# Optimization experiments

Hardware: AMD Instinct MI355X
Metric: run time of the kernel (lower is better)

The kernel has to match this reference:

```python
import jax, jax.numpy as jnp
import numpy as np

B, V, NV, NR, N, E, D, H, OUT, L = 4, 20, 8000, 200, 8000, 200000, 128, 128, 64, 3
DECAY = 0.03


def setup_inputs() -> dict:
    key = jax.random.key(0)
    ks = jax.random.split(key, 16)
    node_ids = jax.random.randint(ks[0], (N,), 0, NV)
    rel_ids = jax.random.randint(ks[1], (E,), 0, NR)
    edge_index = jax.random.randint(ks[2], (2, E), 0, N)
    batch = jnp.repeat(jnp.arange(B), N // B)  # sorted graph assignment, 2000 nodes/graph
    visit_node = (jax.random.uniform(ks[3], (B, V, NV)) < 0.3).astype(jnp.float32)
    ehr_nodes = (jax.random.uniform(ks[4], (B, NV)) < 0.1).astype(jnp.float32)
    s = lambda k, shape: jax.random.normal(k, shape, jnp.float32) * 0.05
    return dict(
        node_ids=node_ids, rel_ids=rel_ids, edge_index=edge_index, batch=batch,
        visit_node=visit_node, ehr_nodes=ehr_nodes,
        node_emb_w=s(ks[5], (NV, D)), rel_emb_w=s(ks[6], (NR, D)),
        lin_w=s(ks[7], (D, H)), lin_b=jnp.zeros((H,), jnp.float32),
        alpha_w=s(ks[8], (L, H)), alpha_b=jnp.zeros((L,), jnp.float32),
        beta_w=s(ks[9], (L, NV)), beta_b=jnp.zeros((L,), jnp.float32),
        conv_w=s(ks[10], (L, H, H)), conv_b=jnp.zeros((L, H), jnp.float32),
        wr_w=s(ks[11], (L, H)), wr_b=jnp.zeros((L,), jnp.float32),
        mlp_w=s(ks[12], (2 * H, OUT)), mlp_b=jnp.zeros((OUT,), jnp.float32),
    )


def reference(node_ids, rel_ids, edge_index, batch, visit_node, ehr_nodes,
              node_emb_w, rel_emb_w, lin_w, lin_b, alpha_w, alpha_b,
              beta_w, beta_b, conv_w, conv_b, wr_w, wr_b, mlp_w, mlp_b):
    # shared input projection (torch: self.lin applied to node and edge embeddings)
    x = node_emb_w[node_ids] @ lin_w + lin_b          # [N,H]
    edge_attr = rel_emb_w[rel_ids] @ lin_w + lin_b    # [E,H]

    # pack per-graph node features into dense [B, NV, H] (x_new in torch, fixed across layers)
    counts = jax.ops.segment_sum(jnp.ones((N,), jnp.float32), batch, B)            # [B]
    starts = jnp.concatenate([jnp.zeros((1,), jnp.int32),
                              jnp.cumsum(counts.astype(jnp.int32))[:-1]])
    local = jnp.arange(N) - starts[batch]                                          # position within graph
    x_pad = jnp.zeros((B, NV, H), jnp.float32).at[batch, local].set(x)

    lam = jnp.exp(DECAY * (V - jnp.arange(V, dtype=jnp.float32)))[None, :, None]   # [1,V,1]
    src, dst = edge_index[0], edge_index[1]
    eb, en = batch[src], node_ids[src]

    for l in range(L):
        # alpha attention over visits (softmax on visit axis)
        feat = visit_node[..., None] * x_pad[:, None]                              # [B,V,NV,H]
        alpha = jax.nn.softmax(jnp.einsum('bvnh,h->bvn', feat, alpha_w[l]) + alpha_b[l], axis=1)
        # beta: time-decayed visit attention
        beta = jnp.tanh(visit_node @ beta_w[l] + beta_b[l])[:, :, None] * lam      # [B,V,1]
        attn_full = alpha * beta                                                   # [B,V,NV]
        attn_e = attn_full[eb, 0, en][:, None]                                     # [E,1] (visit idx 0 as in source)
        # BiAttentionGNNConv: gather-mul-relu-scatter with edge attention
        w_rel = (edge_attr @ wr_w[l] + wr_b[l])[:, None]                           # [E,1]
        msg = jax.nn.relu(x[src] * attn_e + w_rel * edge_attr)                     # [E,H]
        agg = jax.ops.segment_sum(msg, dst, N)                                     # scatter-add to targets
        x = jax.nn.relu((agg + x) @ conv_w[l] + conv_b[l])                         # eps=0 -> (1+eps)*x = x; dropout=eval

    # joint patient representation
    x_graph = jax.ops.segment_sum(x, batch, B) / counts[:, None]                   # global mean pool
    x_node = (ehr_nodes @ node_emb_w) / jnp.sum(ehr_nodes, axis=1, keepdims=True)  # [B,D]
    x_node = x_node @ lin_w + lin_b
    logits = jnp.concatenate([x_graph, x_node], axis=1) @ mlp_w + mlp_b            # [B,OUT]
    return logits
```

## Files before the change

kernel.cpp:

```cpp
#include <hip/hip_runtime.h>

#define NN  8000
#define EE  200000
#define BB  4
#define VV  20
#define NVV 8000
#define NRR 200
#define HH  128
#define OO  64
#define LL  3

__global__ void k_zero_small(float* p, int n) {
  int i = blockIdx.x * 256 + threadIdx.x;
  if (i < n) p[i] = 0.f;
}
__global__ void k_zero_int(int* p, int n) {
  int i = blockIdx.x * 256 + threadIdx.x;
  if (i < n) p[i] = 0;
}

__global__ __launch_bounds__(128) void k_proj_nodes(
    const int* __restrict__ node_ids, const float* __restrict__ emb,
    const float* __restrict__ lin_w, const float* __restrict__ lin_b,
    const float* __restrict__ alpha_w, float* __restrict__ x,
    float* __restrict__ snode)
{
  int i = blockIdx.x, t = threadIdx.x;
  __shared__ float row[HH];
  __shared__ float part[LL][2];
  row[t] = emb[node_ids[i] * HH + t];
  __syncthreads();
  float acc = lin_b[t];
  #pragma unroll 4
  for (int d = 0; d < HH; ++d) acc += row[d] * lin_w[d * HH + t];
  x[i * HH + t] = acc;
  #pragma unroll
  for (int l = 0; l < LL; ++l) {
    float v = acc * alpha_w[l * HH + t];
    for (int off = 32; off > 0; off >>= 1) v += __shfl_down(v, off, 64);
    if ((t & 63) == 0) part[l][t >> 6] = v;
  }
  __syncthreads();
  if (t == 0) {
    #pragma unroll
    for (int l = 0; l < LL; ++l) snode[l * NN + i] = part[l][0] + part[l][1];
  }
}

__global__ __launch_bounds__(128) void k_proj_rels(
    const float* __restrict__ rel_emb, const float* __restrict__ lin_w,
    const float* __restrict__ lin_b, const float* __restrict__ wr_w,
    const float* __restrict__ wr_b, float* __restrict__ relp,
    float* __restrict__ reldot)
{
  int r = blockIdx.x, t = threadIdx.x;
  __shared__ float row[HH];
  __shared__ float part[LL][2];
  row[t] = rel_emb[r * HH + t];
  __syncthreads();
  float acc = lin_b[t];
  #pragma unroll 4
  for (int d = 0; d < HH; ++d) acc += row[d] * lin_w[d * HH + t];
  relp[r * HH + t] = acc;
  #pragma unroll
  for (int l = 0; l < LL; ++l) {
    float v = acc * wr_w[l * HH + t];
    for (int off = 32; off > 0; off >>= 1) v += __shfl_down(v, off, 64);
    if ((t & 63) == 0) part[l][t >> 6] = v;
  }
  __syncthreads();
  if (t == 0) {
    #pragma unroll
    for (int l = 0; l < LL; ++l) reldot[l * NRR + r] = part[l][0] + part[l][1] + wr_b[l];
  }
}

__global__ __launch_bounds__(256) void k_beta(
    const float* __restrict__ visit_node, const float* __restrict__ beta_w,
    const float* __restrict__ beta_b, float* __restrict__ beta0)
{
  int l = blockIdx.x >> 2, b = blockIdx.x & 3, t = threadIdx.x;
  __shared__ float red[256];
  float acc = 0.f;
  for (int n = t; n < NVV; n += 256)
    acc += visit_node[(b * VV + 0) * NVV + n] * beta_w[l * NVV + n];
  red[t] = acc;
  __syncthreads();
  for (int s = 128; s > 0; s >>= 1) {
    if (t < s) red[t] += red[t + s];
    __syncthreads();
  }
  if (t == 0) beta0[l * BB + b] = tanhf(red[0] + beta_b[l]) * expf(0.03f * 20.0f);
}

__global__ __launch_bounds__(256) void k_attn(
    const float* __restrict__ visit_node, const float* __restrict__ snode,
    const float* __restrict__ alpha_b, const float* __restrict__ beta0,
    float* __restrict__ attn0)
{
  int idx = blockIdx.x * 256 + threadIdx.x;
  if (idx >= BB * NVV) return;
  int b = idx / NVV, n = idx % NVV;
  float vn[VV];
  #pragma unroll
  for (int v = 0; v < VV; ++v) vn[v] = visit_node[(b * VV + v) * NVV + n];
  for (int l = 0; l < LL; ++l) {
    float s = (n < NN / BB) ? snode[l * NN + b * (NN / BB) + n] : 0.0f;
    float ab = alpha_b[l];
    float m = -1e30f;
    #pragma unroll
    for (int v = 0; v < VV; ++v) m = fmaxf(m, vn[v] * s + ab);
    float sum = 0.f;
    #pragma unroll
    for (int v = 0; v < VV; ++v) sum += expf(vn[v] * s + ab - m);
    float a0 = expf(vn[0] * s + ab - m) / sum;
    attn0[(l * BB + b) * NVV + n] = a0 * beta0[l * BB + b];
  }
}

__global__ void k_anode(const int* __restrict__ node_ids, const int* __restrict__ batch,
                        const float* __restrict__ attn0, float* __restrict__ anode)
{
  int i = blockIdx.x * 256 + threadIdx.x;
  if (i >= NN) return;
  int b = batch[i], nid = node_ids[i];
  #pragma unroll
  for (int l = 0; l < LL; ++l) anode[l * NN + i] = attn0[(l * BB + b) * NVV + nid];
}

__global__ void k_hist(const int* __restrict__ edge_index, int* __restrict__ deg) {
  int e = blockIdx.x * 256 + threadIdx.x;
  if (e >= EE) return;
  atomicAdd(&deg[edge_index[EE + e]], 1);
}

__global__ __launch_bounds__(1024) void k_scan(const int* __restrict__ deg,
                                               int* __restrict__ row_ptr)
{
  int t = threadIdx.x;
  __shared__ int ps[1024];
  int local[8];
  int base = t * 8;
  int s = 0;
  #pragma unroll
  for (int j = 0; j < 8; ++j) {
    int idx = base + j;
    int v = (idx < NN) ? deg[idx] : 0;
    local[j] = s; s += v;
  }
  ps[t] = s;
  __syncthreads();
  for (int off = 1; off < 1024; off <<= 1) {
    int v = (t >= off) ? ps[t - off] : 0;
    __syncthreads();
    ps[t] += v;
    __syncthreads();
  }
  int excl = (t == 0) ? 0 : ps[t - 1];
  #pragma unroll
  for (int j = 0; j < 8; ++j) {
    int idx = base + j;
    if (idx < NN) row_ptr[idx] = excl + local[j];
  }
  if (t == 1023) row_ptr[NN] = ps[1023];
}

__global__ void k_scatter(const int* __restrict__ edge_index, const int* __restrict__ rel_ids,
                          const int* __restrict__ row_ptr, int* __restrict__ cursor,
                          int* __restrict__ csr_src, int* __restrict__ csr_rid)
{
  int e = blockIdx.x * 256 + threadIdx.x;
  if (e >= EE) return;
  int dst = edge_index[EE + e];
  int p = row_ptr[dst] + atomicAdd(&cursor[dst], 1);
  csr_src[p] = edge_index[e];
  csr_rid[p] = rel_ids[e];
}

__global__ __launch_bounds__(128) void k_gather_conv(
    const int* __restrict__ row_ptr, const int* __restrict__ csr_src,
    const int* __restrict__ csr_rid, const float* __restrict__ xin,
    const float* __restrict__ relp, const float* __restrict__ anode,
    const float* __restrict__ reldot, const float* __restrict__ conv_w,
    const float* __restrict__ conv_b, float* __restrict__ xout, int l)
{
  int i = blockIdx.x, t = threadIdx.x;
  __shared__ float wl[NRR];
  __shared__ float aggrow[HH];
  for (int r = t; r < NRR; r += HH) wl[r] = reldot[l * NRR + r];
  __syncthreads();
  float acc = xin[i * HH + t];
  int k0 = row_ptr[i], k1 = row_ptr[i + 1];
  for (int k = k0; k < k1; ++k) {
    int src = csr_src[k];
    int rid = csr_rid[k];
    float a = anode[l * NN + src];
    acc += fmaxf(xin[src * HH + t] * a + wl[rid] * relp[rid * HH + t], 0.f);
  }
  aggrow[t] = acc;
  __syncthreads();
  float o = conv_b[l * HH + t];
  #pragma unroll 4
  for (int d = 0; d < HH; ++d) o += aggrow[d] * conv_w[(l * HH + d) * HH + t];
  xout[i * HH + t] = fmaxf(o, 0.f);
}

__global__ __launch_bounds__(128) void k_xgraph(
    const float* __restrict__ x, float* __restrict__ xg_raw)
{
  int b = blockIdx.x >> 4, c = blockIdx.x & 15, t = threadIdx.x;
  const int per = (NN / BB) / 16;
  int base = b * (NN / BB) + c * per;
  float acc = 0.f;
  for (int i = 0; i < per; ++i) acc += x[(base + i) * HH + t];
  atomicAdd(&xg_raw[b * HH + t], acc);
}

__global__ __launch_bounds__(128) void k_xnode(
    const float* __restrict__ ehr, const float* __restrict__ emb,
    float* __restrict__ xn_raw, float* __restrict__ denom)
{
  int b = blockIdx.x >> 5, c = blockIdx.x & 31, t = threadIdx.x;
  const int per = NVV / 32;
  int base = c * per;
  float acc = 0.f;
  for (int n = base; n < base + per; ++n)
    acc += ehr[b * NVV + n] * emb[n * HH + t];
  atomicAdd(&xn_raw[b * HH + t], acc);
  __shared__ float red[128];
  float dsum = 0.f;
  for (int n = base + t; n < base + per; n += 128) dsum += ehr[b * NVV + n];
  red[t] = dsum;
  __syncthreads();
  for (int s = 64; s > 0; s >>= 1) {
    if (t < s) red[t] += red[t + s];
    __syncthreads();
  }
  if (t == 0) atomicAdd(&denom[b], red[0]);
}

__global__ __launch_bounds__(128) void k_final(
    const float* __restrict__ xg_raw, const float* __restrict__ xn_raw,
    const float* __restrict__ denom, const float* __restrict__ lin_w,
    const float* __restrict__ lin_b, const float* __restrict__ mlp_w,
    const float* __restrict__ mlp_b, float* __restrict__ out)
{
  int b = blockIdx.x, t = threadIdx.x;
  __shared__ float xg[HH], xn[HH], xnp[HH];
  xg[t] = xg_raw[b * HH + t] * (1.0f / (NN / BB));
  xn[t] = xn_raw[b * HH + t] / denom[b];
  __syncthreads();
  float a3 = lin_b[t];
  #pragma unroll 4
  for (int d = 0; d < HH; ++d) a3 += xn[d] * lin_w[d * HH + t];
  xnp[t] = a3;
  __syncthreads();
  if (t < OO) {
    float a4 = mlp_b[t];
    #pragma unroll 4
    for (int h = 0; h < HH; ++h)
      a4 += xg[h] * mlp_w[h * OO + t] + xnp[h] * mlp_w[(HH + h) * OO + t];
    out[b * OO + t] = a4;
  }
}

extern "C" void kernel_launch(void* const* d_in, const int* in_sizes, int n_in,
                              void* d_out, int out_size, void* d_ws, size_t ws_size,
                              hipStream_t stream) {
  const int*   node_ids   = (const int*)d_in[0];
  const int*   rel_ids    = (const int*)d_in[1];
  const int*   edge_index = (const int*)d_in[2];
  const int*   batch      = (const int*)d_in[3];
  const float* visit_node = (const float*)d_in[4];
  const float* ehr        = (const float*)d_in[5];
  const float* node_emb   = (const float*)d_in[6];
  const float* rel_emb    = (const float*)d_in[7];
  const float* lin_w      = (const float*)d_in[8];
  const float* lin_b      = (const float*)d_in[9];
  const float* alpha_w    = (const float*)d_in[10];
  const float* alpha_b    = (const float*)d_in[11];
  const float* beta_w     = (const float*)d_in[12];
  const float* beta_b     = (const float*)d_in[13];
  const float* conv_w     = (const float*)d_in[14];
  const float* conv_b     = (const float*)d_in[15];
  const float* wr_w       = (const float*)d_in[16];
  const float* wr_b       = (const float*)d_in[17];
  const float* mlp_w      = (const float*)d_in[18];
  const float* mlp_b      = (const float*)d_in[19];
  float* out = (float*)d_out;

  float* ws = (float*)d_ws;
  float* xA     = ws; ws += NN * HH;
  float* xB     = ws; ws += NN * HH;
  float* relp   = ws; ws += NRR * HH;
  float* reldot = ws; ws += LL * NRR;
  float* snode  = ws; ws += LL * NN;
  float* beta0  = ws; ws += LL * BB;
  float* attn0  = ws; ws += LL * BB * NVV;
  float* anode  = ws; ws += LL * NN;
  float* xg_raw = ws; ws += BB * HH;
  float* xn_raw = ws; ws += BB * HH;
  float* denom  = ws; ws += BB;
  int* iws      = (int*)ws;
  int* deg      = iws; iws += NN;
  int* cursor   = iws; iws += NN;
  int* row_ptr  = iws; iws += NN + 1;
  int* csr_src  = iws; iws += EE;
  int* csr_rid  = iws; iws += EE;

  int nsmall = BB * HH * 2 + BB;
  hipLaunchKernelGGL(k_zero_small, dim3((nsmall + 255) / 256), dim3(256), 0, stream,
                     xg_raw, nsmall);
  hipLaunchKernelGGL(k_zero_int, dim3((2 * NN + 255) / 256), dim3(256), 0, stream,
                     deg, 2 * NN);

  hipLaunchKernelGGL(k_proj_nodes, dim3(NN), dim3(HH), 0, stream,
                     node_ids, node_emb, lin_w, lin_b, alpha_w, xA, snode);
  hipLaunchKernelGGL(k_proj_rels, dim3(NRR), dim3(HH), 0, stream,
                     rel_emb, lin_w, lin_b, wr_w, wr_b, relp, reldot);
  hipLaunchKernelGGL(k_beta, dim3(LL * BB), dim3(256), 0, stream,
                     visit_node, beta_w, beta_b, beta0);
  hipLaunchKernelGGL(k_attn, dim3((BB * NVV + 255) / 256), dim3(256), 0, stream,
                     visit_node, snode, alpha_b, beta0, attn0);
  hipLaunchKernelGGL(k_anode, dim3((NN + 255) / 256), dim3(256), 0, stream,
                     node_ids, batch, attn0, anode);

  hipLaunchKernelGGL(k_hist, dim3((EE + 255) / 256), dim3(256), 0, stream,
                     edge_index, deg);
  hipLaunchKernelGGL(k_scan, dim3(1), dim3(1024), 0, stream, deg, row_ptr);
  hipLaunchKernelGGL(k_scatter, dim3((EE + 255) / 256), dim3(256), 0, stream,
                     edge_index, rel_ids, row_ptr, cursor, csr_src, csr_rid);

  const float* xin = xA;
  float* xout = xB;
  for (int l = 0; l < LL; ++l) {
    hipLaunchKernelGGL(k_gather_conv, dim3(NN), dim3(HH), 0, stream,
                       row_ptr, csr_src, csr_rid, xin, relp, anode, reldot,
                       conv_w, conv_b, xout, l);
    const float* tmp = xin; xin = xout; xout = (float*)tmp;
  }

  hipLaunchKernelGGL(k_xgraph, dim3(BB * 16), dim3(HH), 0, stream, xB, xg_raw);
  hipLaunchKernelGGL(k_xnode, dim3(BB * 32), dim3(HH), 0, stream,
                     ehr, node_emb, xn_raw, denom);
  hipLaunchKernelGGL(k_final, dim3(BB), dim3(HH), 0, stream,
                     xg_raw, xn_raw, denom, lin_w, lin_b, mlp_w, mlp_b, out);
}
```

Before: 358.9 us.

## Batch nodes per block, vectorize gather-conv, precompute per-edge attention and relation terms

The gather-conv kernel now handles 8 nodes per 256-thread block, with 32 lanes per node using float4 loads. The edge loop is unrolled by two, and the conv weights are reused across the 8 nodes. Relation terms are premultiplied per layer (wr·relp), and per-edge attention values are precomputed into CSR order during the scatter, which removes indirect loads from the inner loop. Node projection also processes 8 nodes per block to reuse lin_w, and the two zeroing kernels are merged. In exchange it uses more workspace and lowers the thread count per node, and the beta multiply moves into k_anode.

Result: faster. 320.7 us (-10.7%).

```diff
diff --git a/kernel.cpp b/kernel.cpp
--- a/kernel.cpp
+++ b/kernel.cpp
@@ -9,14 +9,12 @@
 #define HH  128
 #define OO  64
 #define LL  3
-
-__global__ void k_zero_small(float* p, int n) {
+#define NPB 8
+
+__global__ void k_zero(float* fz, int nf, int* iz, int ni) {
   int i = blockIdx.x * 256 + threadIdx.x;
-  if (i < n) p[i] = 0.f;
-}
-__global__ void k_zero_int(int* p, int n) {
-  int i = blockIdx.x * 256 + threadIdx.x;
-  if (i < n) p[i] = 0;
+  if (i < nf) fz[i] = 0.f;
+  if (i < ni) iz[i] = 0;
 }
 
 __global__ __launch_bounds__(128) void k_proj_nodes(
@@ -25,33 +23,55 @@
     const float* __restrict__ alpha_w, float* __restrict__ x,
     float* __restrict__ snode)
 {
-  int i = blockIdx.x, t = threadIdx.x;
-  __shared__ float row[HH];
-  __shared__ float part[LL][2];
-  row[t] = emb[node_ids[i] * HH + t];
-  __syncthreads();
-  float acc = lin_b[t];
-  #pragma unroll 4
-  for (int d = 0; d < HH; ++d) acc += row[d] * lin_w[d * HH + t];
-  x[i * HH + t] = acc;
+  int blk = blockIdx.x, t = threadIdx.x;
+  __shared__ float er[NPB][HH];
+  __shared__ float part[LL][NPB][2];
+  int base = blk * NPB;
+  #pragma unroll
+  for (int n = 0; n < NPB; ++n)
+    er[n][t] = emb[node_ids[base + n] * HH + t];
+  __syncthreads();
+  float bt = lin_b[t];
+  float acc[NPB];
+  #pragma unroll
+  for (int n = 0; n < NPB; ++n) acc[n] = bt;
+  for (int d4 = 0; d4 < HH / 4; ++d4) {
+    float e4[NPB][4];
+    #pragma unroll
+    for (int n = 0; n < NPB; ++n) {
+      float4 v = *(const float4*)&er[n][d4 * 4];
+      e4[n][0] = v.x; e4[n][1] = v.y; e4[n][2] = v.z; e4[n][3] = v.w;
+    }
+    #pragma unroll
+    for (int j = 0; j < 4; ++j) {
+      float lwv = lin_w[(d4 * 4 + j) * HH + t];
+      #pragma unroll
+      for (int n = 0; n < NPB; ++n) acc[n] += e4[n][j] * lwv;
+    }
+  }
+  #pragma unroll
+  for (int n = 0; n < NPB; ++n) x[(base + n) * HH + t] = acc[n];
   #pragma unroll
   for (int l = 0; l < LL; ++l) {
-    float v = acc * alpha_w[l * HH + t];
-    for (int off = 32; off > 0; off >>= 1) v += __shfl_down(v, off, 64);
-    if ((t & 63) == 0) part[l][t >> 6] = v;
-  }
-  __syncthreads();
-  if (t == 0) {
+    float aw = alpha_w[l * HH + t];
     #pragma unroll
-    for (int l = 0; l < LL; ++l) snode[l * NN + i] = part[l][0] + part[l][1];
+    for (int n = 0; n < NPB; ++n) {
+      float v = acc[n] * aw;
+      for (int off = 32; off > 0; off >>= 1) v += __shfl_down(v, off, 64);
+      if ((t & 63) == 0) part[l][n][t >> 6] = v;
+    }
+  }
+  __syncthreads();
+  if (t < LL * NPB) {
+    int l = t / NPB, n = t % NPB;
+    snode[l * NN + base + n] = part[l][n][0] + part[l][n][1];
   }
 }
 
 __global__ __launch_bounds__(128) void k_proj_rels(
     const float* __restrict__ rel_emb, const float* __restrict__ lin_w,
     const float* __restrict__ lin_b, const float* __restrict__ wr_w,
-    const float* __restrict__ wr_b, float* __restrict__ relp,
-    float* __restrict__ reldot)
+    const float* __restrict__ wr_b, float* __restrict__ wrelp)
 {
   int r = blockIdx.x, t = threadIdx.x;
   __shared__ float row[HH];
@@ -61,7 +81,6 @@
   float acc = lin_b[t];
   #pragma unroll 4
   for (int d = 0; d < HH; ++d) acc += row[d] * lin_w[d * HH + t];
-  relp[r * HH + t] = acc;
   #pragma unroll
   for (int l = 0; l < LL; ++l) {
     float v = acc * wr_w[l * HH + t];
@@ -69,9 +88,10 @@
     if ((t & 63) == 0) part[l][t >> 6] = v;
   }
   __syncthreads();
-  if (t == 0) {
-    #pragma unroll
-    for (int l = 0; l < LL; ++l) reldot[l * NRR + r] = part[l][0] + part[l][1] + wr_b[l];
+  #pragma unroll
+  for (int l = 0; l < LL; ++l) {
+    float rd = part[l][0] + part[l][1] + wr_b[l];
+    wrelp[(l * NRR + r) * HH + t] = rd * acc;
   }
 }
 
@@ -95,8 +115,7 @@
 
 __global__ __launch_bounds__(256) void k_attn(
     const float* __restrict__ visit_node, const float* __restrict__ snode,
-    const float* __restrict__ alpha_b, const float* __restrict__ beta0,
-    float* __restrict__ attn0)
+    const float* __restrict__ alpha_b, float* __restrict__ attn0)
 {
   int idx = blockIdx.x * 256 + threadIdx.x;
   if (idx >= BB * NVV) return;
@@ -113,19 +132,20 @@
     float sum = 0.f;
     #pragma unroll
     for (int v = 0; v < VV; ++v) sum += expf(vn[v] * s + ab - m);
-    float a0 = expf(vn[0] * s + ab - m) / sum;
-    attn0[(l * BB + b) * NVV + n] = a0 * beta0[l * BB + b];
+    attn0[(l * BB + b) * NVV + n] = expf(vn[0] * s + ab - m) / sum;
   }
 }
 
 __global__ void k_anode(const int* __restrict__ node_ids, const int* __restrict__ batch,
-                        const float* __restrict__ attn0, float* __restrict__ anode)
+                        const float* __restrict__ attn0, const float* __restrict__ beta0,
+                        float* __restrict__ anode)
 {
   int i = blockIdx.x * 256 + threadIdx.x;
   if (i >= NN) return;
   int b = batch[i], nid = node_ids[i];
   #pragma unroll
-  for (int l = 0; l < LL; ++l) anode[l * NN + i] = attn0[(l * BB + b) * NVV + nid];
+  for (int l = 0; l < LL; ++l)
+    anode[l * NN + i] = attn0[(l * BB + b) * NVV + nid] * beta0[l * BB + b];
 }
 
 __global__ void k_hist(const int* __restrict__ edge_index, int* __restrict__ deg) {
@@ -167,42 +187,80 @@
 
 __global__ void k_scatter(const int* __restrict__ edge_index, const int* __restrict__ rel_ids,
                           const int* __restrict__ row_ptr, int* __restrict__ cursor,
-                          int* __restrict__ csr_src, int* __restrict__ csr_rid)
+                          int2* __restrict__ csr_sr, float* __restrict__ csr_a,
+                          const float* __restrict__ anode)
 {
   int e = blockIdx.x * 256 + threadIdx.x;
   if (e >= EE) return;
+  int src = edge_index[e];
   int dst = edge_index[EE + e];
+  int rid = rel_ids[e];
   int p = row_ptr[dst] + atomicAdd(&cursor[dst], 1);
-  csr_src[p] = edge_index[e];
-  csr_rid[p] = rel_ids[e];
-}
-
-__global__ __launch_bounds__(128) void k_gather_conv(
-    const int* __restrict__ row_ptr, const int* __restrict__ csr_src,
-    const int* __restrict__ csr_rid, const float* __restrict__ xin,
-    const float* __restrict__ relp, const float* __restrict__ anode,
-    const float* __restrict__ reldot, const float* __restrict__ conv_w,
+  csr_sr[p] = make_int2(src, rid);
+  csr_a[0 * EE + p] = anode[0 * NN + src];
+  csr_a[1 * EE + p] = anode[1 * NN + src];
+  csr_a[2 * EE + p] = anode[2 * NN + src];
+}
+
+__global__ __launch_bounds__(256) void k_gather_conv(
+    const int* __restrict__ row_ptr, const int2* __restrict__ csr_sr,
+    const float* __restrict__ csr_a, const float* __restrict__ xin,
+    const float* __restrict__ wrelp, const float* __restrict__ conv_w,
     const float* __restrict__ conv_b, float* __restrict__ xout, int l)
 {
-  int i = blockIdx.x, t = threadIdx.x;
-  __shared__ float wl[NRR];
-  __shared__ float aggrow[HH];
-  for (int r = t; r < NRR; r += HH) wl[r] = reldot[l * NRR + r];
-  __syncthreads();
-  float acc = xin[i * HH + t];
+  int t = threadIdx.x;
+  int sub = t >> 5, lane = t & 31;
+  int i = blockIdx.x * NPB + sub;
+  __shared__ float aggrow[NPB][HH];
+  const float4* __restrict__ xin4 = (const float4*)xin;
+  const float4* __restrict__ wr4 = (const float4*)wrelp + (size_t)l * NRR * 32;
+  const float4* __restrict__ cw4 = (const float4*)conv_w + (size_t)l * HH * 32;
+  const float* __restrict__ ca = csr_a + (size_t)l * EE;
+
+  float4 acc = xin4[i * 32 + lane];
   int k0 = row_ptr[i], k1 = row_ptr[i + 1];
-  for (int k = k0; k < k1; ++k) {
-    int src = csr_src[k];
-    int rid = csr_rid[k];
-    float a = anode[l * NN + src];
-    acc += fmaxf(xin[src * HH + t] * a + wl[rid] * relp[rid * HH + t], 0.f);
-  }
-  aggrow[t] = acc;
-  __syncthreads();
-  float o = conv_b[l * HH + t];
-  #pragma unroll 4
-  for (int d = 0; d < HH; ++d) o += aggrow[d] * conv_w[(l * HH + d) * HH + t];
-  xout[i * HH + t] = fmaxf(o, 0.f);
+  int k = k0;
+  for (; k + 1 < k1; k += 2) {
+    int2 sr0 = csr_sr[k];
+    int2 sr1 = csr_sr[k + 1];
+    float a0 = ca[k], a1 = ca[k + 1];
+    float4 x0 = xin4[sr0.x * 32 + lane];
+    float4 w0 = wr4[sr0.y * 32 + lane];
+    float4 x1 = xin4[sr1.x * 32 + lane];
+    float4 w1 = wr4[sr1.y * 32 + lane];
+    acc.x += fmaxf(x0.x * a0 + w0.x, 0.f) + fmaxf(x1.x * a1 + w1.x, 0.f);
+    acc.y += fmaxf(x0.y * a0 + w0.y, 0.f) + fmaxf(x1.y * a1 + w1.y, 0.f);
+    acc.z += fmaxf(x0.z * a0 + w0.z, 0.f) + fmaxf(x1.z * a1 + w1.z, 0.f);
+    acc.w += fmaxf(x0.w * a0 + w0.w, 0.f) + fmaxf(x1.w * a1 + w1.w, 0.f);
+  }
+  if (k < k1) {
+    int2 sr0 = csr_sr[k];
+    float a0 = ca[k];
+    float4 x0 = xin4[sr0.x * 32 + lane];
+    float4 w0 = wr4[sr0.y * 32 + lane];
+    acc.x += fmaxf(x0.x * a0 + w0.x, 0.f);
+    acc.y += fmaxf(x0.y * a0 + w0.y, 0.f);
+    acc.z += fmaxf(x0.z * a0 + w0.z, 0.f);
+    acc.w += fmaxf(x0.w * a0 + w0.w, 0.f);
+  }
+  *(float4*)&aggrow[sub][lane * 4] = acc;
+  __syncthreads();
+
+  float4 o = ((const float4*)conv_b)[l * 32 + lane];
+  for (int d4 = 0; d4 < HH / 4; ++d4) {
+    float4 ag = *(const float4*)&aggrow[sub][d4 * 4];
+    float4 c0 = cw4[(d4 * 4 + 0) * 32 + lane];
+    float4 c1 = cw4[(d4 * 4 + 1) * 32 + lane];
+    float4 c2 = cw4[(d4 * 4 + 2) * 32 + lane];
+    float4 c3 = cw4[(d4 * 4 + 3) * 32 + lane];
+    o.x += ag.x * c0.x + ag.y * c1.x + ag.z * c2.x + ag.w * c3.x;
+    o.y += ag.x * c0.y + ag.y * c1.y + ag.z * c2.y + ag.w * c3.y;
+    o.z += ag.x * c0.z + ag.y * c1.z + ag.z * c2.z + ag.w * c3.z;
+    o.w += ag.x * c0.w + ag.y * c1.w + ag.z * c2.w + ag.w * c3.w;
+  }
+  o.x = fmaxf(o.x, 0.f); o.y = fmaxf(o.y, 0.f);
+  o.z = fmaxf(o.z, 0.f); o.w = fmaxf(o.w, 0.f);
+  ((float4*)xout)[i * 32 + lane] = o;
 }
 
 __global__ __launch_bounds__(128) void k_xgraph(
@@ -292,8 +350,7 @@
   float* ws = (float*)d_ws;
   float* xA     = ws; ws += NN * HH;
   float* xB     = ws; ws += NN * HH;
-  float* relp   = ws; ws += NRR * HH;
-  float* reldot = ws; ws += LL * NRR;
+  float* wrelp  = ws; ws += LL * NRR * HH;
   float* snode  = ws; ws += LL * NN;
   float* beta0  = ws; ws += LL * BB;
   float* attn0  = ws; ws += LL * BB * NVV;
@@ -304,39 +361,37 @@
   int* iws      = (int*)ws;
   int* deg      = iws; iws += NN;
   int* cursor   = iws; iws += NN;
-  int* row_ptr  = iws; iws += NN + 1;
-  int* csr_src  = iws; iws += EE;
-  int* csr_rid  = iws; iws += EE;
-
-  int nsmall = BB * HH * 2 + BB;
-  hipLaunchKernelGGL(k_zero_small, dim3((nsmall + 255) / 256), dim3(256), 0, stream,
-                     xg_raw, nsmall);
-  hipLaunchKernelGGL(k_zero_int, dim3((2 * NN + 255) / 256), dim3(256), 0, stream,
-                     deg, 2 * NN);
-
-  hipLaunchKernelGGL(k_proj_nodes, dim3(NN), dim3(HH), 0, stream,
+  int* row_ptr  = iws; iws += NN + 2;
+  int2* csr_sr  = (int2*)iws; iws += 2 * EE;
+  float* csr_a  = (float*)iws;
+
+  int nf = BB * HH * 2 + BB;
+  int ni = 2 * NN;
+  hipLaunchKernelGGL(k_zero, dim3((ni + 255) / 256), dim3(256), 0, stream,
+                     xg_raw, nf, deg, ni);
+
+  hipLaunchKernelGGL(k_proj_nodes, dim3(NN / NPB), dim3(HH), 0, stream,
                      node_ids, node_emb, lin_w, lin_b, alpha_w, xA, snode);
   hipLaunchKernelGGL(k_proj_rels, dim3(NRR), dim3(HH), 0, stream,
-                     rel_emb, lin_w, lin_b, wr_w, wr_b, relp, reldot);
+                     rel_emb, lin_w, lin_b, wr_w, wr_b, wrelp);
   hipLaunchKernelGGL(k_beta, dim3(LL * BB), dim3(256), 0, stream,
                      visit_node, beta_w, beta_b, beta0);
   hipLaunchKernelGGL(k_attn, dim3((BB * NVV + 255) / 256), dim3(256), 0, stream,
-                     visit_node, snode, alpha_b, beta0, attn0);
+                     visit_node, snode, alpha_b, attn0);
   hipLaunchKernelGGL(k_anode, dim3((NN + 255) / 256), dim3(256), 0, stream,
-                     node_ids, batch, attn0, anode);
+                     node_ids, batch, attn0, beta0, anode);
 
   hipLaunchKernelGGL(k_hist, dim3((EE + 255) / 256), dim3(256), 0, stream,
                      edge_index, deg);
   hipLaunchKernelGGL(k_scan, dim3(1), dim3(1024), 0, stream, deg, row_ptr);
   hipLaunchKernelGGL(k_scatter, dim3((EE + 255) / 256), dim3(256), 0, stream,
-                     edge_index, rel_ids, row_ptr, cursor, csr_src, csr_rid);
+                     edge_index, rel_ids, row_ptr, cursor, csr_sr, csr_a, anode);
 
   const float* xin = xA;
   float* xout = xB;
   for (int l = 0; l < LL; ++l) {
-    hipLaunchKernelGGL(k_gather_conv, dim3(NN), dim3(HH), 0, stream,
-                       row_ptr, csr_src, csr_rid, xin, relp, anode, reldot,
-                       conv_w, conv_b, xout, l);
+    hipLaunchKernelGGL(k_gather_conv, dim3(NN / NPB), dim3(256), 0, stream,
+                       row_ptr, csr_sr, csr_a, xin, wrelp, conv_w, conv_b, xout, l);
     const float* tmp = xin; xin = xout; xout = (float*)tmp;
   }
 
```
